# Optimization experiments

Measured on AMD Instinct MI355X. Metric: run time of the kernel, lower is better.

## Reference

```python
import jax, jax.numpy as jnp
import numpy as np

B, I, H = 16384, 1024, 1024
LN_EPS = 1e-5


def setup_inputs() -> dict:
    key = jax.random.key(0)
    k1, k2, k3, k4 = jax.random.split(key, 4)
    x = jax.random.normal(k1, (B, I), dtype=jnp.float32)
    h_out = jax.random.normal(k2, (B, H), dtype=jnp.float32)
    cell = jax.random.normal(k3, (B, H), dtype=jnp.float32)
    # nn.Linear(i_size + h, 4*h, bias=False): weight shape [4h, i+h]
    W = jax.random.normal(k4, (4 * H, I + H), dtype=jnp.float32) * (1.0 / np.sqrt(I + H))
    gamma = jnp.ones((4, H), dtype=jnp.float32)
    beta = jnp.zeros((4, H), dtype=jnp.float32)
    return {"x": x, "h_out": h_out, "cell": cell, "W": W, "gamma": gamma, "beta": beta}


def reference(x, h_out, cell, W, gamma, beta):
    # concat + linear -> [B, 4, H]
    cat = jnp.concatenate([x, h_out], axis=-1)               # [B, I+H]
    t = (cat @ W.T).reshape(cat.shape[0], 4, H)              # [B, 4, H]
    # LayerNorm over normalized_shape=(4, H): stats over last two dims
    mu = jnp.mean(t, axis=(-2, -1), keepdims=True)
    var = jnp.mean(jnp.square(t - mu), axis=(-2, -1), keepdims=True)
    handle = (t - mu) * jax.lax.rsqrt(var + LN_EPS) * gamma + beta
    # gates: first 3 slices sigmoid, last slice GELU (exact, eval-mode dropout = identity)
    gates = jax.nn.sigmoid(handle[:, 0:3, :])
    f_gate, i_gate, o_gate = gates[:, 0], gates[:, 1], gates[:, 2]
    h_cand = jax.nn.gelu(handle[:, 3, :], approximate=False)
    new_cell = f_gate * cell + i_gate * h_cand
    new_out = o_gate * new_cell
    return (new_out, new_cell)
```

## Files before the change

### kernel.cpp

```cpp
#include <hip/hip_runtime.h>
#include <stdint.h>

#define B_ROWS 16384
#define IN_DIM 1024
#define H_DIM  1024
#define KDIM   2048
#define NDIM   4096
#define NT     64
#define LN_EPSF 1e-5f

typedef unsigned short u16;
typedef float  f32x4  __attribute__((ext_vector_type(4)));
typedef float  fv4    __attribute__((ext_vector_type(4)));
typedef __bf16 bf16x8 __attribute__((ext_vector_type(8)));
typedef u16    u16x4  __attribute__((ext_vector_type(4)));
typedef u16    u16x8  __attribute__((ext_vector_type(8)));

__device__ __forceinline__ u16 f2bf(float f) {
  unsigned u = __float_as_uint(f);
  u += 0x7FFFu + ((u >> 16) & 1u);
  return (u16)(u >> 16);
}
__device__ __forceinline__ float bf2f(u16 s) {
  return __uint_as_float(((unsigned)s) << 16);
}

#define GLOAD_LDS16(gp, lp) __builtin_amdgcn_global_load_lds( \
    (__attribute__((address_space(1))) void*)(gp),            \
    (__attribute__((address_space(3))) void*)(lp), 16, 0, 0)

__global__ __launch_bounds__(256) void cast_concat(
    const float* __restrict__ x, const float* __restrict__ h,
    u16* __restrict__ cat) {
  int idx = blockIdx.x * 256 + threadIdx.x;
  long base = (long)idx * 8;
  int  c = (int)(base & (KDIM - 1));
  long b = base >> 11;
  const float* src = (c < IN_DIM) ? (x + b * IN_DIM + c)
                                  : (h + b * H_DIM + (c - IN_DIM));
  fv4 v0 = *(const fv4*)(src);
  fv4 v1 = *(const fv4*)(src + 4);
  u16x8 o;
  o[0]=f2bf(v0[0]); o[1]=f2bf(v0[1]); o[2]=f2bf(v0[2]); o[3]=f2bf(v0[3]);
  o[4]=f2bf(v1[0]); o[5]=f2bf(v1[1]); o[6]=f2bf(v1[2]); o[7]=f2bf(v1[3]);
  *(u16x8*)(cat + base) = o;
}

__global__ __launch_bounds__(256) void cast_plain(
    const float* __restrict__ w, u16* __restrict__ wb) {
  int idx = blockIdx.x * 256 + threadIdx.x;
  long base = (long)idx * 8;
  fv4 v0 = *(const fv4*)(w + base);
  fv4 v1 = *(const fv4*)(w + base + 4);
  u16x8 o;
  o[0]=f2bf(v0[0]); o[1]=f2bf(v0[1]); o[2]=f2bf(v0[2]); o[3]=f2bf(v0[3]);
  o[4]=f2bf(v1[0]); o[5]=f2bf(v1[1]); o[6]=f2bf(v1[2]); o[7]=f2bf(v1[3]);
  *(u16x8*)(wb + base) = o;
}


__global__ __launch_bounds__(512, 2) void gemm_bt(
    const u16* __restrict__ A,
    const u16* __restrict__ Bw,
    u16* __restrict__ C) {
  __shared__ u16 As[4][8192];
  __shared__ u16 Bs[4][8192];

  const int tid  = threadIdx.x;
  const int lane = tid & 63;
  const int wave = tid >> 6;
  const int wm   = wave >> 2;
  const int wn   = wave & 3;
  const int r    = lane & 15;
  const int g    = lane >> 4;

  const int bid = blockIdx.x;
  const int xcd = bid & 7;
  const int k_  = bid >> 3;
  const int row0 = (xcd * 8 + (k_ >> 4)) * 256;
  const int col0 = (k_ & 15) * 256;

  const int tid2 = tid ^ ((tid >> 3) & 7);
  const u16* gA0 = A  + (size_t)(row0 + (tid2 >> 2)) * KDIM + (tid2 & 3) * 8;
  const u16* gA1 = gA0 + (size_t)128 * KDIM;
  const u16* gB0 = Bw + (size_t)(col0 + (tid2 >> 2)) * KDIM + (tid2 & 3) * 8;
  const u16* gB1 = gB0 + (size_t)128 * KDIM;

  const int rswz   = ((r >> 1) & 7) << 3;
  const int base_a = (((wm * 128 + r) * 32) + g * 8) ^ rswz;
  const int base_b = (((wn * 64  + r) * 32) + g * 8) ^ rswz;

  f32x4 acc[8][4] = {};

#pragma unroll
  for (int tt = 0; tt < 3; ++tt) {
    GLOAD_LDS16(gA0 + tt * 32, &As[tt][tid * 8]);
    GLOAD_LDS16(gA1 + tt * 32, &As[tt][tid * 8 + 4096]);
    GLOAD_LDS16(gB0 + tt * 32, &Bs[tt][tid * 8]);
    GLOAD_LDS16(gB1 + tt * 32, &Bs[tt][tid * 8 + 4096]);
  }
  asm volatile("s_waitcnt vmcnt(8)" ::: "memory");
  __builtin_amdgcn_s_barrier();

#pragma unroll 4
  for (int t = 0; t < NT; ++t) {
    const u16* __restrict__ ab = &As[0][0] + (t & 3) * 8192;
    const u16* __restrict__ bb = &Bs[0][0] + (t & 3) * 8192;
    u16* __restrict__ sa = &As[0][0] + ((t + 3) & 3) * 8192;
    u16* __restrict__ sb = &Bs[0][0] + ((t + 3) & 3) * 8192;
    const bool st = (t + 3) < NT;
    const size_t tso = (size_t)(t + 3) * 32;
    bf16x8 fa[8], fb[4];

#pragma unroll
    for (int i = 0; i < 4; ++i) {
      fb[i] = *(const bf16x8*)(bb + base_b + i * 512);
      fa[i] = *(const bf16x8*)(ab + base_a + i * 512);
    }
    if (st) {
      GLOAD_LDS16(gA0 + tso, sa + tid * 8);
      GLOAD_LDS16(gA1 + tso, sa + tid * 8 + 4096);
    }
    __builtin_amdgcn_s_barrier();
    asm volatile("s_waitcnt lgkmcnt(0)" ::: "memory");
    __builtin_amdgcn_sched_barrier(0);
    __builtin_amdgcn_s_setprio(1);
#pragma unroll
    for (int m = 0; m < 4; ++m)
#pragma unroll
      for (int n = 0; n < 4; ++n)
        acc[m][n] = __builtin_amdgcn_mfma_f32_16x16x32_bf16(
            fa[m], fb[n], acc[m][n], 0, 0, 0);
    __builtin_amdgcn_s_setprio(0);
    __builtin_amdgcn_sched_barrier(0);
    __builtin_amdgcn_s_barrier();

#pragma unroll
    for (int i = 4; i < 8; ++i)
      fa[i] = *(const bf16x8*)(ab + base_a + i * 512);
    if (st) {
      GLOAD_LDS16(gB0 + tso, sb + tid * 8);
      GLOAD_LDS16(gB1 + tso, sb + tid * 8 + 4096);
    }
    __builtin_amdgcn_s_barrier();
    asm volatile("s_waitcnt lgkmcnt(0)" ::: "memory");
    __builtin_amdgcn_sched_barrier(0);
    __builtin_amdgcn_s_setprio(1);
#pragma unroll
    for (int m = 4; m < 8; ++m)
#pragma unroll
      for (int n = 0; n < 4; ++n)
        acc[m][n] = __builtin_amdgcn_mfma_f32_16x16x32_bf16(
            fa[m], fb[n], acc[m][n], 0, 0, 0);
    __builtin_amdgcn_s_setprio(0);
    __builtin_amdgcn_sched_barrier(0);
    if (st) { asm volatile("s_waitcnt vmcnt(8)" ::: "memory"); }
    else    { asm volatile("s_waitcnt vmcnt(0)" ::: "memory"); }
    __builtin_amdgcn_s_barrier();
  }

#pragma unroll
  for (int m = 0; m < 8; ++m)
#pragma unroll
    for (int n = 0; n < 4; ++n)
#pragma unroll
      for (int q = 0; q < 4; ++q) {
        const int rr = row0 + wm * 128 + m * 16 + g * 4 + q;
        const int cc = col0 + wn * 64 + n * 16 + r;
        C[(size_t)rr * NDIM + cc] = f2bf(acc[m][n][q]);
      }
}

__global__ __launch_bounds__(256) void ln_gates(
    const u16* __restrict__ t,
    const float* __restrict__ cell,
    const float* __restrict__ gamma,
    const float* __restrict__ beta,
    float* __restrict__ out) {
  const int b   = blockIdx.x;
  const int tid = threadIdx.x;
  const int h0  = tid * 4;

  const u16* trow = t + (long)b * NDIM;
  float v[4][4];
#pragma unroll
  for (int gi = 0; gi < 4; ++gi) {
    u16x4 raw = *(const u16x4*)&trow[gi * H_DIM + h0];
#pragma unroll
    for (int j = 0; j < 4; ++j) v[gi][j] = bf2f(raw[j]);
  }

  float s1 = 0.f, s2 = 0.f;
#pragma unroll
  for (int gi = 0; gi < 4; ++gi)
#pragma unroll
    for (int j = 0; j < 4; ++j) { s1 += v[gi][j]; s2 += v[gi][j] * v[gi][j]; }

#pragma unroll
  for (int m = 32; m; m >>= 1) {
    s1 += __shfl_xor(s1, m);
    s2 += __shfl_xor(s2, m);
  }
  __shared__ float red[2][4];
  const int wave = tid >> 6, lane = tid & 63;
  if (lane == 0) { red[0][wave] = s1; red[1][wave] = s2; }
  __syncthreads();
  s1 = red[0][0] + red[0][1] + red[0][2] + red[0][3];
  s2 = red[1][0] + red[1][1] + red[1][2] + red[1][3];

  const float mean  = s1 * (1.f / (float)NDIM);
  const float var   = s2 * (1.f / (float)NDIM) - mean * mean;
  const float scale = rsqrtf(var + LN_EPSF);

  float hd[4][4];
#pragma unroll
  for (int gi = 0; gi < 4; ++gi) {
    fv4 gm = *(const fv4*)&gamma[gi * H_DIM + h0];
    fv4 bt = *(const fv4*)&beta[gi * H_DIM + h0];
#pragma unroll
    for (int j = 0; j < 4; ++j)
      hd[gi][j] = (v[gi][j] - mean) * scale * gm[j] + bt[j];
  }

  fv4 cv = *(const fv4*)&cell[(long)b * H_DIM + h0];
  fv4 no, nc;
#pragma unroll
  for (int j = 0; j < 4; ++j) {
    float fg = 1.f / (1.f + expf(-hd[0][j]));
    float ig = 1.f / (1.f + expf(-hd[1][j]));
    float og = 1.f / (1.f + expf(-hd[2][j]));
    float hc = 0.5f * hd[3][j] * (1.f + erff(hd[3][j] * 0.70710678118654752f));
    float ncell = fg * cv[j] + ig * hc;
    nc[j] = ncell;
    no[j] = og * ncell;
  }
  *(fv4*)&out[(long)b * H_DIM + h0] = no;
  *(fv4*)&out[(long)B_ROWS * H_DIM + (long)b * H_DIM + h0] = nc;
}

extern "C" void kernel_launch(void* const* d_in, const int* in_sizes, int n_in,
                              void* d_out, int out_size, void* d_ws, size_t ws_size,
                              hipStream_t stream) {
  const float* x     = (const float*)d_in[0];
  const float* h     = (const float*)d_in[1];
  const float* cell  = (const float*)d_in[2];
  const float* W     = (const float*)d_in[3];
  const float* gamma = (const float*)d_in[4];
  const float* beta  = (const float*)d_in[5];
  float* out = (float*)d_out;

  const size_t cat_bytes = (size_t)B_ROWS * KDIM * sizeof(u16);
  const size_t w_bytes   = (size_t)NDIM * KDIM * sizeof(u16);
  const size_t t_bytes   = (size_t)B_ROWS * NDIM * sizeof(u16);
  if (ws_size < cat_bytes + w_bytes + t_bytes) return;

  uint8_t* ws = (uint8_t*)d_ws;
  u16* catb = (u16*)ws;
  u16* Wb   = (u16*)(ws + cat_bytes);
  u16* tbuf = (u16*)(ws + cat_bytes + w_bytes);

  cast_concat<<<(B_ROWS * (long)KDIM / 8) / 256, 256, 0, stream>>>(x, h, catb);
  cast_plain<<<(NDIM * (long)KDIM / 8) / 256, 256, 0, stream>>>(W, Wb);

  gemm_bt<<<dim3(1024), 512, 0, stream>>>(catb, Wb, tbuf);

  ln_gates<<<B_ROWS, 256, 0, stream>>>(tbuf, cell, gamma, beta, out);
}
```

Before: 382.9 us.

## Restructure GEMM main loop into 8-phase ping-pong schedule with K=64 tiles

Replaces the 4-stage K=32 LDS ring with a 2-buffer K=64 layout and a hand-scheduled 8-phase loop. Each phase interleaves LDS fragment reads, partial global-to-LDS loads and a quarter of the MFMA work, with a new XOR swizzle for the wider rows. The goal is better overlap of loads with MFMA and fewer barriers per unit of K work. In exchange it brings tighter vmcnt/lgkmcnt bookkeeping, where any miscount would cause races, and it keeps more fragment registers live.

After: 364.7 us. -4.7%, faster.

```diff
diff --git a/kernel.cpp b/kernel.cpp
--- a/kernel.cpp
+++ b/kernel.cpp
@@ -6,7 +6,6 @@
 #define H_DIM  1024
 #define KDIM   2048
 #define NDIM   4096
-#define NT     64
 #define LN_EPSF 1e-5f
 
 typedef unsigned short u16;
@@ -59,12 +58,47 @@
 }
 
 
+#define STA(S_, P_, T_) GLOAD_LDS16(pA + (size_t)(P_) * 64 * KDIM + (T_) * 64, \
+                                    &LA[S_][(P_) * 4096 + tid * 8])
+#define STB(S_, P_, T_) GLOAD_LDS16(pB + (size_t)(P_) * 64 * KDIM + (T_) * 64, \
+                                    &LB[S_][(P_) * 4096 + tid * 8])
+
+#define RDA(S_, MB_) { const u16* ap = &LA[S_][abase + ((MB_) >> 2) * 4096];  \
+  _Pragma("unroll") for (int i_ = 0; i_ < 4; ++i_) {                          \
+    a[i_][0] = *(const bf16x8*)(ap + i_ * 1024 + kk0);                        \
+    a[i_][1] = *(const bf16x8*)(ap + i_ * 1024 + kk1); } }
+
+#define RDB(S_, V_, NB_) { const u16* bp = &LB[S_][bbase + (NB_) * 1024];     \
+  _Pragma("unroll") for (int i_ = 0; i_ < 2; ++i_) {                          \
+    V_[i_][0] = *(const bf16x8*)(bp + i_ * 1024 + kk0);                       \
+    V_[i_][1] = *(const bf16x8*)(bp + i_ * 1024 + kk1); } }
+
+#define MQ(MB_, NB_, V_)                                                      \
+  _Pragma("unroll") for (int m_ = 0; m_ < 4; ++m_)                            \
+  _Pragma("unroll") for (int n_ = 0; n_ < 2; ++n_) {                          \
+    acc[(MB_) + m_][(NB_) + n_] = __builtin_amdgcn_mfma_f32_16x16x32_bf16(    \
+        a[m_][0], V_[n_][0], acc[(MB_) + m_][(NB_) + n_], 0, 0, 0);           \
+    acc[(MB_) + m_][(NB_) + n_] = __builtin_amdgcn_mfma_f32_16x16x32_bf16(    \
+        a[m_][1], V_[n_][1], acc[(MB_) + m_][(NB_) + n_], 0, 0, 0); }
+
+#define HEAD                                                                  \
+  __builtin_amdgcn_sched_barrier(0);                                          \
+  __builtin_amdgcn_s_barrier();                                               \
+  asm volatile("s_waitcnt lgkmcnt(0)" ::: "memory");                          \
+  __builtin_amdgcn_sched_barrier(0);                                          \
+  __builtin_amdgcn_s_setprio(1);
+
+#define TAIL                                                                  \
+  __builtin_amdgcn_s_setprio(0);                                              \
+  __builtin_amdgcn_sched_barrier(0);                                          \
+  __builtin_amdgcn_s_barrier();
+
 __global__ __launch_bounds__(512, 2) void gemm_bt(
     const u16* __restrict__ A,
     const u16* __restrict__ Bw,
     u16* __restrict__ C) {
-  __shared__ u16 As[4][8192];
-  __shared__ u16 Bs[4][8192];
+  __shared__ u16 LA[2][16384];
+  __shared__ u16 LB[2][16384];
 
   const int tid  = threadIdx.x;
   const int lane = tid & 63;
@@ -80,82 +114,71 @@
   const int row0 = (xcd * 8 + (k_ >> 4)) * 256;
   const int col0 = (k_ & 15) * 256;
 
-  const int tid2 = tid ^ ((tid >> 3) & 7);
-  const u16* gA0 = A  + (size_t)(row0 + (tid2 >> 2)) * KDIM + (tid2 & 3) * 8;
-  const u16* gA1 = gA0 + (size_t)128 * KDIM;
-  const u16* gB0 = Bw + (size_t)(col0 + (tid2 >> 2)) * KDIM + (tid2 & 3) * 8;
-  const u16* gB1 = gB0 + (size_t)128 * KDIM;
-
-  const int rswz   = ((r >> 1) & 7) << 3;
-  const int base_a = (((wm * 128 + r) * 32) + g * 8) ^ rswz;
-  const int base_b = (((wn * 64  + r) * 32) + g * 8) ^ rswz;
+  const int l    = tid ^ ((tid >> 3) & 7);
+  const int srow = l >> 3;
+  const int skc  = (l & 7) * 8;
+  const u16* pA = A  + (size_t)(row0 + srow) * KDIM + skc;
+  const u16* pB = Bw + (size_t)(col0 + srow) * KDIM + skc;
+
+  const int rx   = r & 7;
+  const int kk0  = ((g      ) ^ rx) << 3;
+  const int kk1  = (((4 | g)) ^ rx) << 3;
+  const int abase = wm * 8192 + r * 64;
+  const int bbase = wn * 4096 + r * 64;
 
   f32x4 acc[8][4] = {};
-
-#pragma unroll
-  for (int tt = 0; tt < 3; ++tt) {
-    GLOAD_LDS16(gA0 + tt * 32, &As[tt][tid * 8]);
-    GLOAD_LDS16(gA1 + tt * 32, &As[tt][tid * 8 + 4096]);
-    GLOAD_LDS16(gB0 + tt * 32, &Bs[tt][tid * 8]);
-    GLOAD_LDS16(gB1 + tt * 32, &Bs[tt][tid * 8 + 4096]);
-  }
-  asm volatile("s_waitcnt vmcnt(8)" ::: "memory");
+  bf16x8 a[4][2], b0[2][2], b1[2][2];
+
+  STA(0, 0, 0); STA(0, 1, 0); STA(0, 2, 0); STA(0, 3, 0);
+  STB(0, 0, 0); STB(0, 1, 0); STB(0, 2, 0); STB(0, 3, 0);
+  STA(1, 0, 1); STA(1, 2, 1);
+  STB(1, 0, 1); STB(1, 1, 1); STB(1, 2, 1); STB(1, 3, 1);
+  asm volatile("s_waitcnt vmcnt(6)" ::: "memory");
   __builtin_amdgcn_s_barrier();
 
-#pragma unroll 4
-  for (int t = 0; t < NT; ++t) {
-    const u16* __restrict__ ab = &As[0][0] + (t & 3) * 8192;
-    const u16* __restrict__ bb = &Bs[0][0] + (t & 3) * 8192;
-    u16* __restrict__ sa = &As[0][0] + ((t + 3) & 3) * 8192;
-    u16* __restrict__ sb = &Bs[0][0] + ((t + 3) & 3) * 8192;
-    const bool st = (t + 3) < NT;
-    const size_t tso = (size_t)(t + 3) * 32;
-    bf16x8 fa[8], fb[4];
-
-#pragma unroll
-    for (int i = 0; i < 4; ++i) {
-      fb[i] = *(const bf16x8*)(bb + base_b + i * 512);
-      fa[i] = *(const bf16x8*)(ab + base_a + i * 512);
-    }
-    if (st) {
-      GLOAD_LDS16(gA0 + tso, sa + tid * 8);
-      GLOAD_LDS16(gA1 + tso, sa + tid * 8 + 4096);
-    }
-    __builtin_amdgcn_s_barrier();
-    asm volatile("s_waitcnt lgkmcnt(0)" ::: "memory");
-    __builtin_amdgcn_sched_barrier(0);
-    __builtin_amdgcn_s_setprio(1);
-#pragma unroll
-    for (int m = 0; m < 4; ++m)
-#pragma unroll
-      for (int n = 0; n < 4; ++n)
-        acc[m][n] = __builtin_amdgcn_mfma_f32_16x16x32_bf16(
-            fa[m], fb[n], acc[m][n], 0, 0, 0);
+  for (int it = 0; it < 16; ++it) {
+    const int u = 2 * it;
+    const bool st = it < 15;
+
+    RDA(0, 0); RDB(0, b0, 0);
+    STA(1, 1, u + 1); STA(1, 3, u + 1);
+    asm volatile("s_waitcnt lgkmcnt(8)" ::: "memory");
+    HEAD; MQ(0, 0, b0); TAIL;
+
+    RDB(0, b1, 2);
+    if (st) { STA(0, 0, u + 2); STA(0, 2, u + 2); }
+    HEAD; MQ(0, 2, b1); TAIL;
+
+    RDA(0, 4);
+    if (st) { STB(0, 0, u + 2); STB(0, 1, u + 2); }
+    HEAD; MQ(4, 0, b0); TAIL;
+
+    if (st) { STB(0, 2, u + 2); STB(0, 3, u + 2); }
+    HEAD; MQ(4, 2, b1);
     __builtin_amdgcn_s_setprio(0);
     __builtin_amdgcn_sched_barrier(0);
+    if (st) { asm volatile("s_waitcnt vmcnt(4)" ::: "memory"); }
+    else    { asm volatile("s_waitcnt vmcnt(0)" ::: "memory"); }
     __builtin_amdgcn_s_barrier();
 
-#pragma unroll
-    for (int i = 4; i < 8; ++i)
-      fa[i] = *(const bf16x8*)(ab + base_a + i * 512);
-    if (st) {
-      GLOAD_LDS16(gB0 + tso, sb + tid * 8);
-      GLOAD_LDS16(gB1 + tso, sb + tid * 8 + 4096);
-    }
-    __builtin_amdgcn_s_barrier();
-    asm volatile("s_waitcnt lgkmcnt(0)" ::: "memory");
-    __builtin_amdgcn_sched_barrier(0);
-    __builtin_amdgcn_s_setprio(1);
-#pragma unroll
-    for (int m = 4; m < 8; ++m)
-#pragma unroll
-      for (int n = 0; n < 4; ++n)
-        acc[m][n] = __builtin_amdgcn_mfma_f32_16x16x32_bf16(
-            fa[m], fb[n], acc[m][n], 0, 0, 0);
+    RDA(1, 0); RDB(1, b0, 0);
+    if (st) { STA(0, 1, u + 2); STA(0, 3, u + 2); }
+    asm volatile("s_waitcnt lgkmcnt(8)" ::: "memory");
+    HEAD; MQ(0, 0, b0); TAIL;
+
+    RDB(1, b1, 2);
+    if (st) { STA(1, 0, u + 3); STA(1, 2, u + 3); }
+    HEAD; MQ(0, 2, b1); TAIL;
+
+    RDA(1, 4);
+    if (st) { STB(1, 0, u + 3); STB(1, 1, u + 3); }
+    HEAD; MQ(4, 0, b0); TAIL;
+
+    if (st) { STB(1, 2, u + 3); STB(1, 3, u + 3); }
+    HEAD; MQ(4, 2, b1);
     __builtin_amdgcn_s_setprio(0);
     __builtin_amdgcn_sched_barrier(0);
-    if (st) { asm volatile("s_waitcnt vmcnt(8)" ::: "memory"); }
-    else    { asm volatile("s_waitcnt vmcnt(0)" ::: "memory"); }
+    if (st) { asm volatile("s_waitcnt vmcnt(6)" ::: "memory"); }
     __builtin_amdgcn_s_barrier();
   }
 
```
